# Optimization experiments

Measured on AMD Instinct MI355X. Metric: run time of the kernel, lower is better.

Reference implementation:

```python
import jax, jax.numpy as jnp
import numpy as np

B, N, MAX_DIM = 8, 256, 2
D = 2 + MAX_DIM
EPS = 1e-8


def _lsa(cost):
    """Exact Jonker-Volgenant shortest-augmenting-path assignment (== scipy
    linear_sum_assignment) for a square cost matrix. Returns col4row."""
    n = cost.shape[0]
    u = np.zeros(n)
    v = np.zeros(n)
    col4row = np.full(n, -1)
    row4col = np.full(n, -1)
    for cur in range(n):
        shortest = np.full(n, np.inf)
        path = np.full(n, -1)
        SR = np.zeros(n, bool)
        SC = np.zeros(n, bool)
        i = cur
        minVal = 0.0
        sink = -1
        while sink == -1:
            SR[i] = True
            d = minVal + cost[i] - u[i] - v
            upd = (~SC) & (d < shortest)
            shortest[upd] = d[upd]
            path[upd] = i
            j = int(np.argmin(np.where(SC, np.inf, shortest)))
            minVal = shortest[j]
            SC[j] = True
            if row4col[j] == -1:
                sink = j
            else:
                i = row4col[j]
        u[cur] += minVal
        sr = SR.copy()
        sr[cur] = False
        ridx = np.where(sr)[0]
        u[ridx] += minVal - shortest[col4row[ridx]]
        cidx = np.where(SC)[0]
        v[cidx] -= minVal - shortest[cidx]
        j = sink
        while True:
            i = path[j]
            row4col[j] = i
            col4row[i], j = j, col4row[i]
            if i == cur:
                break
    return col4row


def _proj(p):
    # project point onto the diagonal midpoint: x' = x + sqrt(y+eps)/2, y' = 0
    return p[..., 0] + jnp.sqrt(p[..., 1] + EPS) / 2.0


def _dim_dist(set1, set2, dim):
    # NOTE: the torch code aliases set*_cur and set*_cur_projected, so the
    # in-place projection zeroes the y-coordinate of BOTH halves of each
    # concatenation. Hence every point is (proj_x, 0) and cdist(p=2)
    # degenerates to |x_a - x_b|. We reproduce that math faithfully.
    labels = jnp.argmax(set2[:, :, 2:], axis=2)                      # [B,N]
    s2 = (set2 * (labels == dim)[..., None])[:, :, :2]               # [B,N,2]
    s1 = (set1 * (set1[:, :, 2] == dim)[..., None])[:, :, :2]        # [B,N,2]
    p1 = _proj(s1)                                                   # [B,N]
    p2 = _proj(s2)                                                   # [B,N]
    a = jnp.concatenate([p1, p2], axis=0)                            # [2B,N]
    b = jnp.concatenate([p2, p1], axis=0)                            # [2B,N]
    return jnp.abs(a[:, :, None] - b[:, None, :])                    # [2B,N,N]


def _match(dist):
    dn = np.asarray(jax.lax.stop_gradient(dist))
    dn = np.where(np.isnan(dn), 1e6, dn)
    return jnp.asarray(np.stack([_lsa(c) for c in dn]))              # [2B,N]


def setup_inputs():
    key = jax.random.key(0)
    k1, k2, k3 = jax.random.split(key, 3)
    set1 = jax.random.uniform(k1, (B, N, D), dtype=jnp.float32)
    dims = jax.random.randint(k3, (B, N), 0, MAX_DIM).astype(jnp.float32)
    set1 = set1.at[:, :, 2].set(dims)  # integer homology-dim labels in col 2
    set2 = jax.random.uniform(k2, (B, N, D), dtype=jnp.float32)
    return {"set1": set1, "set2": set2}


def reference(set1, set2):
    max_dim = set2.shape[2] - 2
    total = jnp.float32(0.0)
    for dim in range(max_dim):
        dist = _dim_dist(set1, set2, dim)   # [2B,N,N]
        cols = _match(dist)                 # [2B,N] Hungarian assignment
        bb = jnp.arange(dist.shape[0])[:, None]
        rr = jnp.arange(dist.shape[1])[None, :]
        total = total + dist[bb, rr, cols].mean(axis=1).sum()
    return total
```

## Files before the change

kernel.cpp:

```cpp
#include <hip/hip_runtime.h>
#include <math.h>

#define PB 8
#define PN 256
#define PD 4
#define PEPS 1e-8f

__global__ __launch_bounds__(256) void hung_partial_kernel(
    const float* __restrict__ set1,
    const float* __restrict__ set2,
    float* __restrict__ partial)
{
    const int blk = blockIdx.x;
    const int dim = blk >> 3;
    const int b   = blk & 7;
    const int tid = threadIdx.x;

    __shared__ float s1[PN];
    __shared__ float s2[PN];

    const float* e1 = set1 + ((size_t)b * PN + tid) * PD;
    const float* e2 = set2 + ((size_t)b * PN + tid) * PD;
    float x1 = e1[0], y1 = e1[1], l1 = e1[2];
    float x2 = e2[0], y2 = e2[1], a2 = e2[2], b2 = e2[3];

    bool m1 = (l1 == (float)dim);
    int lab2 = (b2 > a2) ? 1 : 0;
    bool m2 = (lab2 == dim);

    float mx1 = m1 ? x1 : 0.0f, my1 = m1 ? y1 : 0.0f;
    float mx2 = m2 ? x2 : 0.0f, my2 = m2 ? y2 : 0.0f;

    s1[tid] = mx1 + sqrtf(my1 + PEPS) * 0.5f;
    s2[tid] = mx2 + sqrtf(my2 + PEPS) * 0.5f;
    __syncthreads();

    for (int k = 2; k <= PN; k <<= 1) {
        for (int j = k >> 1; j > 0; j >>= 1) {
            int ixj = tid ^ j;
            if (ixj > tid) {
                bool up = ((tid & k) == 0);
                float a = s1[tid], bb = s1[ixj];
                if ((a > bb) == up) { s1[tid] = bb; s1[ixj] = a; }
                float c = s2[tid], dd = s2[ixj];
                if ((c > dd) == up) { s2[tid] = dd; s2[ixj] = c; }
            }
            __syncthreads();
        }
    }

    float v = fabsf(s1[tid] - s2[tid]);
    #pragma unroll
    for (int off = 32; off > 0; off >>= 1)
        v += __shfl_down(v, off, 64);

    __shared__ float wsum[4];
    int lane = tid & 63, wid = tid >> 6;
    if (lane == 0) wsum[wid] = v;
    __syncthreads();
    if (tid == 0)
        partial[blk] = wsum[0] + wsum[1] + wsum[2] + wsum[3];
}

__global__ void hung_final_kernel(const float* __restrict__ partial,
                                  float* __restrict__ out)
{
    if (threadIdx.x == 0) {
        float s = 0.0f;
        #pragma unroll
        for (int i = 0; i < 16; ++i) s += partial[i];
        out[0] = s * (2.0f / (float)PN);
    }
}

extern "C" void kernel_launch(void* const* d_in, const int* in_sizes, int n_in,
                              void* d_out, int out_size, void* d_ws, size_t ws_size,
                              hipStream_t stream) {
    const float* set1 = (const float*)d_in[0];
    const float* set2 = (const float*)d_in[1];
    float* partial = (float*)d_ws;
    float* out = (float*)d_out;

    hung_partial_kernel<<<16, 256, 0, stream>>>(set1, set2, partial);
    hung_final_kernel<<<1, 64, 0, stream>>>(partial, out);
}
```

Measured before the change: 61.31 us.

## Sort per wave in registers with shuffles and fuse into a single kernel

```diff
diff --git a/kernel.cpp b/kernel.cpp
--- a/kernel.cpp
+++ b/kernel.cpp
@@ -6,69 +6,87 @@
 #define PD 4
 #define PEPS 1e-8f
 
-__global__ __launch_bounds__(256) void hung_partial_kernel(
+
+__device__ __forceinline__ void cmpswap(float& lo, float& hi, bool up) {
+    float mn = fminf(lo, hi);
+    float mx = fmaxf(lo, hi);
+    lo = up ? mn : mx;
+    hi = up ? mx : mn;
+}
+
+__global__ __launch_bounds__(1024) void hung_kernel(
     const float* __restrict__ set1,
     const float* __restrict__ set2,
-    float* __restrict__ partial)
+    float* __restrict__ out)
 {
-    const int blk = blockIdx.x;
-    const int dim = blk >> 3;
-    const int b   = blk & 7;
-    const int tid = threadIdx.x;
+    const int tid  = threadIdx.x;
+    const int wave = tid >> 6;
+    const int lane = tid & 63;
+    const int dim  = wave >> 3;
+    const int b    = wave & 7;
+    const float fdim = (float)dim;
 
-    __shared__ float s1[PN];
-    __shared__ float s2[PN];
+    float p[4];
+    float q[4];
+    const float4* s1v = (const float4*)(set1 + (size_t)b * PN * PD);
+    const float4* s2v = (const float4*)(set2 + (size_t)b * PN * PD);
+    #pragma unroll
+    for (int r = 0; r < 4; ++r) {
+        int n = r * 64 + lane;
+        float4 e1 = s1v[n];
+        float4 e2 = s2v[n];
+        bool m1 = (e1.z == fdim);
+        int lab2 = (e2.w > e2.z) ? 1 : 0;
+        bool m2 = (lab2 == dim);
+        float mx1 = m1 ? e1.x : 0.0f, my1 = m1 ? e1.y : 0.0f;
+        float mx2 = m2 ? e2.x : 0.0f, my2 = m2 ? e2.y : 0.0f;
+        p[r] = mx1 + sqrtf(my1 + PEPS) * 0.5f;
+        q[r] = mx2 + sqrtf(my2 + PEPS) * 0.5f;
+    }
 
-    const float* e1 = set1 + ((size_t)b * PN + tid) * PD;
-    const float* e2 = set2 + ((size_t)b * PN + tid) * PD;
-    float x1 = e1[0], y1 = e1[1], l1 = e1[2];
-    float x2 = e2[0], y2 = e2[1], a2 = e2[2], b2 = e2[3];
-
-    bool m1 = (l1 == (float)dim);
-    int lab2 = (b2 > a2) ? 1 : 0;
-    bool m2 = (lab2 == dim);
-
-    float mx1 = m1 ? x1 : 0.0f, my1 = m1 ? y1 : 0.0f;
-    float mx2 = m2 ? x2 : 0.0f, my2 = m2 ? y2 : 0.0f;
-
-    s1[tid] = mx1 + sqrtf(my1 + PEPS) * 0.5f;
-    s2[tid] = mx2 + sqrtf(my2 + PEPS) * 0.5f;
-    __syncthreads();
-
-    for (int k = 2; k <= PN; k <<= 1) {
+    #pragma unroll
+    for (int k = 2; k <= 256; k <<= 1) {
+        #pragma unroll
         for (int j = k >> 1; j > 0; j >>= 1) {
-            int ixj = tid ^ j;
-            if (ixj > tid) {
-                bool up = ((tid & k) == 0);
-                float a = s1[tid], bb = s1[ixj];
-                if ((a > bb) == up) { s1[tid] = bb; s1[ixj] = a; }
-                float c = s2[tid], dd = s2[ixj];
-                if ((c > dd) == up) { s2[tid] = dd; s2[ixj] = c; }
+            if (j == 128) {
+                cmpswap(p[0], p[2], true);  cmpswap(p[1], p[3], true);
+                cmpswap(q[0], q[2], true);  cmpswap(q[1], q[3], true);
+            } else if (j == 64) {
+                bool up1 = (k == 256);
+                cmpswap(p[0], p[1], true);  cmpswap(p[2], p[3], up1);
+                cmpswap(q[0], q[1], true);  cmpswap(q[2], q[3], up1);
+            } else {
+                bool lower = ((lane & j) == 0);
+                #pragma unroll
+                for (int r = 0; r < 4; ++r) {
+                    int idx = r * 64 + lane;
+                    bool up = ((idx & k) == 0);
+                    bool keepmin = (up == lower);
+                    float po = __shfl_xor(p[r], j, 64);
+                    float qo = __shfl_xor(q[r], j, 64);
+                    float pmn = fminf(p[r], po), pmx = fmaxf(p[r], po);
+                    float qmn = fminf(q[r], qo), qmx = fmaxf(q[r], qo);
+                    p[r] = keepmin ? pmn : pmx;
+                    q[r] = keepmin ? qmn : qmx;
+                }
             }
-            __syncthreads();
         }
     }
 
-    float v = fabsf(s1[tid] - s2[tid]);
+    float v = 0.0f;
+    #pragma unroll
+    for (int r = 0; r < 4; ++r) v += fabsf(p[r] - q[r]);
     #pragma unroll
     for (int off = 32; off > 0; off >>= 1)
-        v += __shfl_down(v, off, 64);
+        v += __shfl_xor(v, off, 64);
 
-    __shared__ float wsum[4];
-    int lane = tid & 63, wid = tid >> 6;
-    if (lane == 0) wsum[wid] = v;
+    __shared__ float wsum[16];
+    if (lane == 0) wsum[wave] = v;
     __syncthreads();
-    if (tid == 0)
-        partial[blk] = wsum[0] + wsum[1] + wsum[2] + wsum[3];
-}
-
-__global__ void hung_final_kernel(const float* __restrict__ partial,
-                                  float* __restrict__ out)
-{
-    if (threadIdx.x == 0) {
+    if (tid == 0) {
         float s = 0.0f;
         #pragma unroll
-        for (int i = 0; i < 16; ++i) s += partial[i];
+        for (int i = 0; i < 16; ++i) s += wsum[i];
         out[0] = s * (2.0f / (float)PN);
     }
 }
@@ -78,9 +96,7 @@
                               hipStream_t stream) {
     const float* set1 = (const float*)d_in[0];
     const float* set2 = (const float*)d_in[1];
-    float* partial = (float*)d_ws;
     float* out = (float*)d_out;
 
-    hung_partial_kernel<<<16, 256, 0, stream>>>(set1, set2, partial);
-    hung_final_kernel<<<1, 64, 0, stream>>>(partial, out);
+    hung_kernel<<<1, 1024, 0, stream>>>(set1, set2, out);
 }
```

Measured after the change: 67.19 us. 9.6% more time.
